# Performance work log

Hardware: AMD Instinct MI355X
Metric: run time of the kernel (lower is better)

## Reference

```python
import jax, jax.numpy as jnp
import numpy as np

DIM = 1024
DEPTH = 2
HEADS = 16
MLP = 4096
HEAD_DIM = DIM // HEADS
EPS = 1e-5


def layernorm(x, w, b):
    mu = jnp.mean(x, axis=-1, keepdims=True)
    var = jnp.mean(jnp.square(x - mu), axis=-1, keepdims=True)
    return (x - mu) * jax.lax.rsqrt(var + EPS) * w + b


def setup_inputs() -> dict:
    key = jax.random.key(0)
    ks = jax.random.split(key, 16)
    s = 0.02
    x = jax.random.normal(ks[0], (2, 2048, DIM), dtype=jnp.float32)
    inp = {
        "x": x,
        "ln1_w": jnp.ones((DEPTH, DIM), jnp.float32),
        "ln1_b": jnp.zeros((DEPTH, DIM), jnp.float32),
        "qkv_w": jax.random.normal(ks[1], (DEPTH, DIM, 3 * DIM), jnp.float32) * s,
        "qkv_b": jnp.zeros((DEPTH, 3 * DIM), jnp.float32),
        "in_w": jax.random.normal(ks[2], (DEPTH, DIM, 3 * DIM), jnp.float32) * s,
        "in_b": jnp.zeros((DEPTH, 3 * DIM), jnp.float32),
        "out_w": jax.random.normal(ks[3], (DEPTH, DIM, DIM), jnp.float32) * s,
        "out_b": jnp.zeros((DEPTH, DIM), jnp.float32),
        "ln2_w": jnp.ones((DEPTH, DIM), jnp.float32),
        "ln2_b": jnp.zeros((DEPTH, DIM), jnp.float32),
        "w1": jax.random.normal(ks[4], (DEPTH, DIM, MLP), jnp.float32) * s,
        "b1": jnp.zeros((DEPTH, MLP), jnp.float32),
        "w2": jax.random.normal(ks[5], (DEPTH, MLP, DIM), jnp.float32) * s,
        "b2": jnp.zeros((DEPTH, DIM), jnp.float32),
    }
    return inp


def _forward(x, ln1_w, ln1_b, qkv_w, qkv_b, in_w, in_b, out_w, out_b,
             ln2_w, ln2_b, w1, b1, w2, b2):
    B, S, D = x.shape
    scale = 1.0 / jnp.sqrt(jnp.float32(HEAD_DIM))
    for i in range(DEPTH):
        # --- Attention block (pre-norm) ---
        h = layernorm(x, ln1_w[i], ln1_b[i])
        qkv = h @ qkv_w[i] + qkv_b[i]                      # [B,S,3D]
        q, k, v = jnp.split(qkv, 3, axis=-1)
        # nn.MultiheadAttention's own in_proj on top of to_qkv
        qp = q @ in_w[i][:, :D] + in_b[i][:D]
        kp = k @ in_w[i][:, D:2 * D] + in_b[i][D:2 * D]
        vp = v @ in_w[i][:, 2 * D:] + in_b[i][2 * D:]
        qp = qp.reshape(B, S, HEADS, HEAD_DIM)
        kp = kp.reshape(B, S, HEADS, HEAD_DIM)
        vp = vp.reshape(B, S, HEADS, HEAD_DIM)
        scores = jnp.einsum("bqhd,bkhd->bhqk", qp, kp) * scale
        attn = jax.nn.softmax(scores, axis=-1)
        o = jnp.einsum("bhqk,bkhd->bqhd", attn, vp).reshape(B, S, D)
        o = o @ out_w[i] + out_b[i]
        x = o + x
        # --- FFN block (pre-norm) ---
        h = layernorm(x, ln2_w[i], ln2_b[i])
        h = jax.nn.gelu(h @ w1[i] + b1[i], approximate=False)
        h = h @ w2[i] + b2[i]
        x = h + x
    return x


def reference(x, ln1_w, ln1_b, qkv_w, qkv_b, in_w, in_b, out_w, out_b,
              ln2_w, ln2_b, w1, b1, w2, b2):
    return _forward(x, ln1_w, ln1_b, qkv_w, qkv_b, in_w, in_b, out_w, out_b,
                    ln2_w, ln2_b, w1, b1, w2, b2)
```

## Files before the change

### kernel.cpp

```cpp
#include <hip/hip_runtime.h>
#include <math.h>

#define D_MODEL 1024
#define NHEADS 16
#define HEAD_DIM 64
#define SEQ 2048
#define BATCH 2
#define TOK (BATCH*SEQ)
#define MLP_DIM 4096

#define F_BIAS  1
#define F_GELU  2
#define QSCALE 0.18033688011112042f

typedef __attribute__((ext_vector_type(8))) __bf16 bf16x8;
typedef __attribute__((ext_vector_type(16))) __bf16 bf16x16;
typedef __attribute__((ext_vector_type(4))) __bf16 bf16x4;
typedef __attribute__((ext_vector_type(4))) float f32x4;

__device__ __forceinline__ void gload16(const void* g, void* l) {
    __builtin_amdgcn_global_load_lds(
        (const __attribute__((address_space(1))) void*)g,
        (__attribute__((address_space(3))) void*)l, 16, 0, 0);
}

__global__ __launch_bounds__(256)
void conv_kernel(const float* __restrict__ in, __bf16* __restrict__ out, int n8)
{
    const int idx = blockIdx.x * 256 + threadIdx.x;
    if (idx >= n8) return;
    const float4 a = *(const float4*)(in + idx * 8);
    const float4 b = *(const float4*)(in + idx * 8 + 4);
    bf16x8 o;
    o[0] = (__bf16)a.x; o[1] = (__bf16)a.y; o[2] = (__bf16)a.z; o[3] = (__bf16)a.w;
    o[4] = (__bf16)b.x; o[5] = (__bf16)b.y; o[6] = (__bf16)b.z; o[7] = (__bf16)b.w;
    *(bf16x8*)(out + idx * 8) = o;
}

__global__ __launch_bounds__(256)
void tconv64_kernel(const float* __restrict__ in, __bf16* __restrict__ out, int R, int C)
{
    __shared__ __bf16 tile[64][72];
    const int bx = blockIdx.x;
    const int by = blockIdx.y;
    const int t = threadIdx.x;
    const int rl = t >> 4, cl = (t & 15) * 4;
    #pragma unroll
    for (int rr = 0; rr < 4; ++rr) {
        const float4 v = *(const float4*)&in[(size_t)(by * 64 + rr * 16 + rl) * C + bx * 64 + cl];
        tile[rr * 16 + rl][cl + 0] = (__bf16)v.x;
        tile[rr * 16 + rl][cl + 1] = (__bf16)v.y;
        tile[rr * 16 + rl][cl + 2] = (__bf16)v.z;
        tile[rr * 16 + rl][cl + 3] = (__bf16)v.w;
    }
    __syncthreads();
    const int oc = t >> 2, rs = (t & 3) * 16;
    bf16x16 y;
    #pragma unroll
    for (int k = 0; k < 16; ++k) y[k] = tile[rs + k][oc];
    *(bf16x16*)&out[(size_t)(bx * 64 + oc) * R + by * 64 + rs] = y;
}

__global__ __launch_bounds__(256)
void bcomb_kernel(const float* __restrict__ qkv_b, const float* __restrict__ in_w,
                  const float* __restrict__ in_b, float* __restrict__ bc)
{
    const int t = blockIdx.x * 256 + threadIdx.x;
    const int p = t >> 10, n = t & 1023;
    float s = in_b[t];
    #pragma unroll 16
    for (int k = 0; k < D_MODEL; ++k)
        s = fmaf(qkv_b[p * D_MODEL + k], in_w[(size_t)k * 3 * D_MODEL + p * D_MODEL + n], s);
    bc[t] = s;
}

__global__ __launch_bounds__(256)
void tv_kernel(const __bf16* __restrict__ v, __bf16* __restrict__ vt)
{
    __shared__ __bf16 t[64][72];
    const int bh = blockIdx.y, b = bh >> 4, h = bh & 15;
    const int s0 = blockIdx.x * 64;
    const int r = threadIdx.x >> 3;
    const int c = (threadIdx.x & 7) * 8;
    #pragma unroll
    for (int rr = 0; rr < 64; rr += 32) {
        bf16x8 x = *(const bf16x8*)&v[(size_t)(b * SEQ + s0 + r + rr) * D_MODEL + h * 64 + c];
        #pragma unroll
        for (int k = 0; k < 8; ++k) t[r + rr][c + k] = x[k];
    }
    __syncthreads();
    #pragma unroll
    for (int rr = 0; rr < 64; rr += 32) {
        bf16x8 y;
        #pragma unroll
        for (int k = 0; k < 8; ++k) y[k] = t[c + k][r + rr];
        *(bf16x8*)&vt[((size_t)bh * 64 + r + rr) * SEQ + s0 + c] = y;
    }
}

__device__ __forceinline__ void ln_body(float4 v, const float* w, const float* b,
                                        __bf16* out, int row, int t)
{
    float s  = v.x + v.y + v.z + v.w;
    float ss = v.x*v.x + v.y*v.y + v.z*v.z + v.w*v.w;
    #pragma unroll
    for (int off = 32; off > 0; off >>= 1) {
        s  += __shfl_down(s, off);
        ss += __shfl_down(ss, off);
    }
    __shared__ float red[8];
    const int wid = t >> 6, lane = t & 63;
    if (lane == 0) { red[wid] = s; red[4 + wid] = ss; }
    __syncthreads();
    const float st  = red[0] + red[1] + red[2] + red[3];
    const float sst = red[4] + red[5] + red[6] + red[7];
    const float mu  = st * (1.0f / D_MODEL);
    const float var = sst * (1.0f / D_MODEL) - mu * mu;
    const float rs  = rsqrtf(var + 1e-5f);
    const float4 wv = *(const float4*)(w + t * 4);
    const float4 bv = *(const float4*)(b + t * 4);
    bf16x4 o;
    o[0] = (__bf16)((v.x - mu) * rs * wv.x + bv.x);
    o[1] = (__bf16)((v.y - mu) * rs * wv.y + bv.y);
    o[2] = (__bf16)((v.z - mu) * rs * wv.z + bv.z);
    o[3] = (__bf16)((v.w - mu) * rs * wv.w + bv.w);
    *(bf16x4*)(out + (size_t)row * D_MODEL + t * 4) = o;
}

__global__ __launch_bounds__(256)
void ln_kernel(const float* __restrict__ x, const float* __restrict__ w,
               const float* __restrict__ b, __bf16* __restrict__ out)
{
    const int row = blockIdx.x, t = threadIdx.x;
    float4 v = *(const float4*)(x + (size_t)row * D_MODEL + t * 4);
    ln_body(v, w, b, out, row, t);
}

__global__ __launch_bounds__(256)
void ln_add_kernel(float* __restrict__ x, const float* __restrict__ p0,
                   const float* __restrict__ p1, const float* __restrict__ w,
                   const float* __restrict__ b, __bf16* __restrict__ out)
{
    const int row = blockIdx.x, t = threadIdx.x;
    const size_t idx = (size_t)row * D_MODEL + t * 4;
    float4 v  = *(const float4*)(x + idx);
    float4 a0 = *(const float4*)(p0 + idx);
    float4 a1 = *(const float4*)(p1 + idx);
    v.x += a0.x + a1.x; v.y += a0.y + a1.y;
    v.z += a0.z + a1.z; v.w += a0.w + a1.w;
    *(float4*)(x + idx) = v;
    ln_body(v, w, b, out, row, t);
}

__global__ __launch_bounds__(256)
void add2_kernel(float* __restrict__ x, const float* __restrict__ p0,
                 const float* __restrict__ p1)
{
    const size_t idx = ((size_t)blockIdx.x * 256 + threadIdx.x) * 4;
    float4 v  = *(const float4*)(x + idx);
    float4 a0 = *(const float4*)(p0 + idx);
    float4 a1 = *(const float4*)(p1 + idx);
    v.x += a0.x + a1.x; v.y += a0.y + a1.y;
    v.z += a0.z + a1.z; v.w += a0.w + a1.w;
    *(float4*)(x + idx) = v;
}

template<int BM, int BN, int WM, int WAVES, int FLAGS, bool PROJ3, bool SPLITK, bool ZB>
__global__ __launch_bounds__(WAVES * 64)
void gs_kernel(const __bf16* __restrict__ A, int lda, long long sAz,
               const __bf16* __restrict__ Bt, int ldb, long long sBz,
               const float* __restrict__ bias,
               void* __restrict__ Cv, int ldc, int K, long long sCz)
{
    constexpr int THREADS = WAVES * 64;
    constexpr int WN = WAVES / WM, RW = BM / WM, CW = BN / WN;
    constexpr int MI = RW / 16, NJ = CW / 16;
    constexpr int LA = (BM * 64) / (THREADS * 8);
    constexpr int LB = (BN * 64) / (THREADS * 8);
    __shared__ __align__(16) __bf16 As[2][BM * 64];
    __shared__ __align__(16) __bf16 Bs[2][BN * 64];

    const int gx = gridDim.x;
    const int nwg = gx * gridDim.y;
    int lin = blockIdx.y * gx + blockIdx.x;
    lin = (lin & 7) * (nwg >> 3) + (lin >> 3);
    const int bm = lin / gx, bn = lin % gx;

    const int z = (SPLITK || ZB) ? blockIdx.z : 0;
    const __bf16* Ab = A  + (size_t)bm * BM * lda
                          + (SPLITK ? (size_t)z * K : 0) + (ZB ? (size_t)z * sAz : 0);
    const __bf16* Bb = Bt + (size_t)bn * BN * ldb
                          + (SPLITK ? (size_t)z * K : 0) + (ZB ? (size_t)z * sBz : 0);

    const int tid = threadIdx.x, lane = tid & 63, w = tid >> 6;
    const int wm = w / WN, wn = w % WN;
    const int kq = lane >> 4, fr = lane & 15;
    const int l8 = lane >> 3;
    const int swz = (lane & 7) ^ l8;

    const __bf16* aPtr[LA]; int aLds[LA];
    #pragma unroll
    for (int c = 0; c < LA; ++c) {
        aPtr[c] = Ab + (size_t)(c * (THREADS / 8) + w * 8 + l8) * lda + swz * 8;
        aLds[c] = (c * THREADS + tid) * 8;
    }
    const __bf16* bPtr[LB]; int bLds[LB];
    #pragma unroll
    for (int c = 0; c < LB; ++c) {
        bPtr[c] = Bb + (size_t)(c * (THREADS / 8) + w * 8 + l8) * ldb + swz * 8;
        bLds[c] = (c * THREADS + tid) * 8;
    }

    f32x4 acc[MI][NJ];
    #pragma unroll
    for (int i = 0; i < MI; ++i)
        #pragma unroll
        for (int j = 0; j < NJ; ++j)
            acc[i][j] = (f32x4){0.f, 0.f, 0.f, 0.f};

    auto STG = [&](int buf, int k0) {
        #pragma unroll
        for (int c = 0; c < LA; ++c)
            gload16(aPtr[c] + k0, &As[buf][aLds[c]]);
        #pragma unroll
        for (int c = 0; c < LB; ++c)
            gload16(bPtr[c] + k0, &Bs[buf][bLds[c]]);
    };

    const int fsw = fr & 7;
    auto COMPUTE = [&](int buf) {
        #pragma unroll
        for (int kk = 0; kk < 2; ++kk) {
            const int kc = (kk * 4 + kq) ^ fsw;
            bf16x8 af[MI], bfr[NJ];
            #pragma unroll
            for (int i = 0; i < MI; ++i)
                af[i] = *(const bf16x8*)&As[buf][(wm * RW + i * 16 + fr) * 64 + kc * 8];
            #pragma unroll
            for (int j = 0; j < NJ; ++j)
                bfr[j] = *(const bf16x8*)&Bs[buf][(wn * CW + j * 16 + fr) * 64 + kc * 8];
            #pragma unroll
            for (int i = 0; i < MI; ++i)
                #pragma unroll
                for (int j = 0; j < NJ; ++j)
                    acc[i][j] = __builtin_amdgcn_mfma_f32_16x16x32_bf16(
                        af[i], bfr[j], acc[i][j], 0, 0, 0);
        }
    };

    const int T = K >> 6;
    STG(0, 0);
    __syncthreads();
    int cur = 0;
    for (int t = 0; t < T; ++t) {
        if (t + 1 < T) STG(cur ^ 1, (t + 1) * 64);
        COMPUTE(cur);
        __syncthreads();
        cur ^= 1;
    }

    const int row0 = bm * BM + wm * RW + kq * 4;
    const int col0 = bn * BN + wn * CW + fr;
    if (SPLITK) {
        float* P = (float*)Cv + (size_t)z * sCz;
        #pragma unroll
        for (int i = 0; i < MI; ++i) {
            #pragma unroll
            for (int j = 0; j < NJ; ++j) {
                const int col = col0 + j * 16;
                const float bb = (z == 0) ? bias[col] : 0.0f;
                #pragma unroll
                for (int e = 0; e < 4; ++e)
                    P[(size_t)(row0 + i * 16 + e) * ldc + col] = acc[i][j][e] + bb;
            }
        }
    } else {
        __bf16* C = (__bf16*)Cv + (ZB ? (size_t)z * sCz : 0);
        #pragma unroll
        for (int i = 0; i < MI; ++i) {
            #pragma unroll
            for (int j = 0; j < NJ; ++j) {
                const int col = col0 + j * 16;
                const float bb = (FLAGS & F_BIAS) ? bias[col] : 0.0f;
                #pragma unroll
                for (int e = 0; e < 4; ++e) {
                    const int row = row0 + i * 16 + e;
                    float val = acc[i][j][e] + bb;
                    if (FLAGS & F_GELU)
                        val = 0.5f * val * (1.0f + erff(val * 0.70710678118654752f));
                    if (PROJ3) {
                        if ((col >> 10) == 0) val *= QSCALE;
                        C[(size_t)(col >> 10) * TOK * D_MODEL +
                          (size_t)row * D_MODEL + (col & 1023)] = (__bf16)val;
                    } else {
                        C[(size_t)row * ldc + col] = (__bf16)val;
                    }
                }
            }
        }
    }
}

__global__ __launch_bounds__(256)
void attn8_kernel(const __bf16* __restrict__ qp, const __bf16* __restrict__ kp,
                  const __bf16* __restrict__ vt, __bf16* __restrict__ o)
{
    const int bh = blockIdx.y;
    const int b = bh >> 4, h = bh & 15;
    const int tid = threadIdx.x;
    const int lane = tid & 63;
    const int w = tid >> 6;
    const int g = lane >> 4;
    const int fr = lane & 15;
    const int q0 = blockIdx.x * 128 + w * 16;
    const int l8 = lane >> 3, swz = (lane & 7) ^ l8, fsw = fr & 7;

    __shared__ __align__(16) __bf16 Ks[2][64 * 64];
    __shared__ __align__(16) __bf16 Vs[2][64 * 64];
    __shared__ __align__(16) __bf16 PsA[4][16 * 72];
    __shared__ __align__(16) __bf16 PsB[4][16 * 72];

    const __bf16* qbA = qp + (size_t)(b * SEQ + q0 + fr) * D_MODEL + h * HEAD_DIM;
    const __bf16* qbB = qbA + (size_t)64 * D_MODEL;
    const bf16x8 qfA0 = *(const bf16x8*)(qbA + g * 8);
    const bf16x8 qfA1 = *(const bf16x8*)(qbA + 32 + g * 8);
    const bf16x8 qfB0 = *(const bf16x8*)(qbB + g * 8);
    const bf16x8 qfB1 = *(const bf16x8*)(qbB + 32 + g * 8);

    const __bf16* kb = kp + (size_t)(b * SEQ) * D_MODEL + h * HEAD_DIM;
    const __bf16* vb = vt + (size_t)bh * HEAD_DIM * SEQ;

    const __bf16* kPtr[2]; const __bf16* vPtr[2]; int sLds[2];
    #pragma unroll
    for (int c = 0; c < 2; ++c) {
        const int row = c * 32 + w * 8 + l8;
        kPtr[c] = kb + (size_t)row * D_MODEL + swz * 8;
        vPtr[c] = vb + (size_t)row * SEQ + swz * 8;
        sLds[c] = (c * 256 + w * 64) * 8;
    }

    auto STG = [&](int buf, int kv0) {
        #pragma unroll
        for (int c = 0; c < 2; ++c)
            gload16(kPtr[c] + (size_t)kv0 * D_MODEL, &Ks[buf][sLds[c]]);
        #pragma unroll
        for (int c = 0; c < 2; ++c)
            gload16(vPtr[c] + kv0, &Vs[buf][sLds[c]]);
    };

    f32x4 acc_oA[4], acc_oB[4];
    #pragma unroll
    for (int dj = 0; dj < 4; ++dj) {
        acc_oA[dj] = (f32x4){0.f, 0.f, 0.f, 0.f};
        acc_oB[dj] = (f32x4){0.f, 0.f, 0.f, 0.f};
    }
    float l_A = 0.0f, l_B = 0.0f;

    STG(0, 0);
    __syncthreads();
    int tb = 0;
    for (int kv0 = 0; kv0 < SEQ; kv0 += 64) {
        if (kv0 + 64 < SEQ) STG(tb ^ 1, kv0 + 64);

        f32x4 sA[4], sB[4];
        __builtin_amdgcn_s_setprio(1);
        #pragma unroll
        for (int t = 0; t < 4; ++t) {
            const bf16x8 kf0 = *(const bf16x8*)&Ks[tb][(t * 16 + fr) * 64 + ((g    ) ^ fsw) * 8];
            const bf16x8 kf1 = *(const bf16x8*)&Ks[tb][(t * 16 + fr) * 64 + ((4 + g) ^ fsw) * 8];
            sA[t] = __builtin_amdgcn_mfma_f32_16x16x32_bf16(
                kf0, qfA0, (f32x4){0.f, 0.f, 0.f, 0.f}, 0, 0, 0);
            sA[t] = __builtin_amdgcn_mfma_f32_16x16x32_bf16(kf1, qfA1, sA[t], 0, 0, 0);
            sB[t] = __builtin_amdgcn_mfma_f32_16x16x32_bf16(
                kf0, qfB0, (f32x4){0.f, 0.f, 0.f, 0.f}, 0, 0, 0);
            sB[t] = __builtin_amdgcn_mfma_f32_16x16x32_bf16(kf1, qfB1, sB[t], 0, 0, 0);
        }
        __builtin_amdgcn_s_setprio(0);

        #pragma unroll
        for (int t = 0; t < 4; ++t) {
            bf16x4 pvA, pvB;
            #pragma unroll
            for (int e = 0; e < 4; ++e) {
                const float pA = __builtin_amdgcn_exp2f(sA[t][e]);
                const float pB = __builtin_amdgcn_exp2f(sB[t][e]);
                l_A += pA; l_B += pB;
                pvA[e] = (__bf16)pA; pvB[e] = (__bf16)pB;
            }
            *(bf16x4*)&PsA[w][fr * 72 + t * 16 + g * 4] = pvA;
            *(bf16x4*)&PsB[w][fr * 72 + t * 16 + g * 4] = pvB;
        }

        __builtin_amdgcn_s_setprio(1);
        #pragma unroll
        for (int c = 0; c < 2; ++c) {
            const bf16x8 pfA = *(const bf16x8*)&PsA[w][fr * 72 + c * 32 + g * 8];
            const bf16x8 pfB = *(const bf16x8*)&PsB[w][fr * 72 + c * 32 + g * 8];
            #pragma unroll
            for (int dj = 0; dj < 4; ++dj) {
                const bf16x8 vf = *(const bf16x8*)&Vs[tb][(dj * 16 + fr) * 64 +
                                                         ((c * 4 + g) ^ fsw) * 8];
                acc_oA[dj] = __builtin_amdgcn_mfma_f32_16x16x32_bf16(vf, pfA, acc_oA[dj], 0, 0, 0);
                acc_oB[dj] = __builtin_amdgcn_mfma_f32_16x16x32_bf16(vf, pfB, acc_oB[dj], 0, 0, 0);
            }
        }
        __builtin_amdgcn_s_setprio(0);
        __syncthreads();
        tb ^= 1;
    }

    l_A += __shfl_xor(l_A, 16); l_A += __shfl_xor(l_A, 32);
    l_B += __shfl_xor(l_B, 16); l_B += __shfl_xor(l_B, 32);
    const float invA = 1.0f / l_A, invB = 1.0f / l_B;
    __bf16* orowA = o + (size_t)(b * SEQ + q0 + fr) * D_MODEL + h * HEAD_DIM;
    __bf16* orowB = orowA + (size_t)64 * D_MODEL;
    #pragma unroll
    for (int dj = 0; dj < 4; ++dj) {
        bf16x4 tA, tB;
        #pragma unroll
        for (int e = 0; e < 4; ++e) {
            tA[e] = (__bf16)(acc_oA[dj][e] * invA);
            tB[e] = (__bf16)(acc_oB[dj][e] * invB);
        }
        *(bf16x4*)&orowA[dj * 16 + g * 4] = tA;
        *(bf16x4*)&orowB[dj * 16 + g * 4] = tB;
    }
}

extern "C" void kernel_launch(void* const* d_in, const int* in_sizes, int n_in,
                              void* d_out, int out_size, void* d_ws, size_t ws_size,
                              hipStream_t stream)
{
    const float* x    = (const float*)d_in[0];
    const float* ln1w = (const float*)d_in[1];
    const float* ln1b = (const float*)d_in[2];
    const float* qkvw = (const float*)d_in[3];
    const float* qkvb = (const float*)d_in[4];
    const float* inw  = (const float*)d_in[5];
    const float* inb  = (const float*)d_in[6];
    const float* outw = (const float*)d_in[7];
    const float* outb = (const float*)d_in[8];
    const float* ln2w = (const float*)d_in[9];
    const float* ln2b = (const float*)d_in[10];
    const float* w1   = (const float*)d_in[11];
    const float* b1   = (const float*)d_in[12];
    const float* w2   = (const float*)d_in[13];
    const float* b2   = (const float*)d_in[14];
    float* xo = (float*)d_out;

    const size_t OFF_WCT = 0;
    const size_t OFF_OUT = 3145728;
    const size_t OFF_W1  = 4194304;
    const size_t OFF_W2  = 8388608;
    const size_t L_WT    = 12582912;

    __bf16* WT   = (__bf16*)d_ws;
    __bf16* QKVb = WT + 2 * L_WT;
    __bf16* INt  = QKVb + 3145728;
    __bf16* X8   = INt + 3145728;
    __bf16* U_   = X8 + 4194304;
    __bf16* QKV3 = U_ + 16777216;
    __bf16* VT   = QKV3 + 12582912;
    float*  BC   = (float*)(VT + 4194304);
    float*  P_   = (float*)QKV3;

    hipMemcpyAsync(xo, x, (size_t)TOK * D_MODEL * sizeof(float),
                   hipMemcpyDeviceToDevice, stream);

    const dim3 blk(256);
    for (int i = 0; i < 2; ++i) {
        __bf16* wl = WT + i * L_WT;
        const float* l_qkvw = qkvw + (size_t)i * D_MODEL * 3 * D_MODEL;
        const float* l_inw  = inw  + (size_t)i * D_MODEL * 3 * D_MODEL;
        conv_kernel<<<1536, blk, 0, stream>>>(l_qkvw, QKVb, 393216);
        tconv64_kernel<<<dim3(48, 16), blk, 0, stream>>>(l_inw, INt, D_MODEL, 3 * D_MODEL);
        gs_kernel<128, 128, 2, 4, 0, false, false, true><<<dim3(8, 8, 3), 256, 0, stream>>>(
            INt, D_MODEL, 1048576LL, QKVb, 3 * D_MODEL, (long long)D_MODEL,
            nullptr, wl + OFF_WCT, D_MODEL, D_MODEL, 1048576LL);
        bcomb_kernel<<<12, blk, 0, stream>>>(
            qkvb + (size_t)i * 3 * D_MODEL, l_inw, inb + (size_t)i * 3 * D_MODEL,
            BC + (size_t)i * 3 * D_MODEL);
        tconv64_kernel<<<dim3(16, 16), blk, 0, stream>>>(
            outw + (size_t)i * D_MODEL * D_MODEL, wl + OFF_OUT, D_MODEL, D_MODEL);
        tconv64_kernel<<<dim3(64, 16), blk, 0, stream>>>(
            w1 + (size_t)i * D_MODEL * MLP_DIM, wl + OFF_W1, D_MODEL, MLP_DIM);
        tconv64_kernel<<<dim3(16, 64), blk, 0, stream>>>(
            w2 + (size_t)i * MLP_DIM * D_MODEL, wl + OFF_W2, MLP_DIM, D_MODEL);
    }

    for (int i = 0; i < 2; ++i) {
        __bf16* wl = WT + i * L_WT;
        const float* l_outb = outb + (size_t)i * D_MODEL;
        const float* l_b1   = b1   + (size_t)i * MLP_DIM;
        const float* l_b2   = b2   + (size_t)i * D_MODEL;

        if (i == 0)
            ln_kernel<<<TOK, blk, 0, stream>>>(xo, ln1w, ln1b, X8);
        gs_kernel<128, 128, 2, 4, F_BIAS, true, false, false><<<dim3(24, 32), 256, 0, stream>>>(
            X8, D_MODEL, 0, wl + OFF_WCT, D_MODEL, 0,
            BC + (size_t)i * 3 * D_MODEL, QKV3, D_MODEL, D_MODEL, 0);
        tv_kernel<<<dim3(SEQ / 64, BATCH * NHEADS), blk, 0, stream>>>(
            QKV3 + (size_t)2 * TOK * D_MODEL, VT);
        attn8_kernel<<<dim3(SEQ / 128, BATCH * NHEADS), blk, 0, stream>>>(
            QKV3, QKV3 + (size_t)TOK * D_MODEL, VT, X8);
        gs_kernel<128, 128, 2, 4, F_BIAS, false, true, false><<<dim3(8, 32, 2), 256, 0, stream>>>(
            X8, D_MODEL, 0, wl + OFF_OUT, D_MODEL, 0, l_outb, P_, D_MODEL, 512,
            (long long)TOK * D_MODEL);
        ln_add_kernel<<<TOK, blk, 0, stream>>>(
            xo, P_, P_ + (size_t)TOK * D_MODEL,
            ln2w + (size_t)i * D_MODEL, ln2b + (size_t)i * D_MODEL, X8);
        gs_kernel<128, 128, 2, 4, F_BIAS | F_GELU, false, false, false><<<dim3(32, 32), 256, 0, stream>>>(
            X8, D_MODEL, 0, wl + OFF_W1, D_MODEL, 0, l_b1, U_, MLP_DIM, D_MODEL, 0);
        gs_kernel<128, 128, 2, 4, F_BIAS, false, true, false><<<dim3(8, 32, 2), 256, 0, stream>>>(
            U_, MLP_DIM, 0, wl + OFF_W2, MLP_DIM, 0, l_b2, P_, D_MODEL, 2048,
            (long long)TOK * D_MODEL);
        if (i == 0) {
            ln_add_kernel<<<TOK, blk, 0, stream>>>(
                xo, P_, P_ + (size_t)TOK * D_MODEL,
                ln1w + D_MODEL, ln1b + D_MODEL, X8);
        } else {
            add2_kernel<<<TOK * D_MODEL / 1024, blk, 0, stream>>>(
                xo, P_, P_ + (size_t)TOK * D_MODEL);
        }
    }
}
```

Measured before the change: 665.1 us.

## Use BK=32 GEMM tiles, split-K by 4 with bf16 partials

Makes the GEMM K-tile size a template parameter and switches every GEMM from BK=64 to BK=32, with a matching LDS swizzle for 32-wide rows. The out-projection and FFN-down GEMMs now use four-way split-K instead of two-way, and their partial sums are stored in bf16 rather than fp32. The residual-add and layernorm kernels read four bf16 partials instead of two fp32 ones. The aims are less LDS per block for higher occupancy, more blocks on the small split-K GEMMs, and less partial-sum traffic. The cost is twice as many K iterations and barriers, plus extra rounding error from bf16 partials.

```diff
diff --git a/kernel.cpp b/kernel.cpp
--- a/kernel.cpp
+++ b/kernel.cpp
@@ -137,35 +137,39 @@
 }
 
 __global__ __launch_bounds__(256)
-void ln_add_kernel(float* __restrict__ x, const float* __restrict__ p0,
-                   const float* __restrict__ p1, const float* __restrict__ w,
-                   const float* __restrict__ b, __bf16* __restrict__ out)
+void ln_add4_kernel(float* __restrict__ x, const __bf16* __restrict__ P,
+                    const float* __restrict__ w, const float* __restrict__ b,
+                    __bf16* __restrict__ out)
 {
     const int row = blockIdx.x, t = threadIdx.x;
     const size_t idx = (size_t)row * D_MODEL + t * 4;
-    float4 v  = *(const float4*)(x + idx);
-    float4 a0 = *(const float4*)(p0 + idx);
-    float4 a1 = *(const float4*)(p1 + idx);
-    v.x += a0.x + a1.x; v.y += a0.y + a1.y;
-    v.z += a0.z + a1.z; v.w += a0.w + a1.w;
+    float4 v = *(const float4*)(x + idx);
+    #pragma unroll
+    for (int z = 0; z < 4; ++z) {
+        const bf16x4 p = *(const bf16x4*)(P + (size_t)z * TOK * D_MODEL + idx);
+        v.x += (float)p[0]; v.y += (float)p[1];
+        v.z += (float)p[2]; v.w += (float)p[3];
+    }
     *(float4*)(x + idx) = v;
     ln_body(v, w, b, out, row, t);
 }
 
 __global__ __launch_bounds__(256)
-void add2_kernel(float* __restrict__ x, const float* __restrict__ p0,
-                 const float* __restrict__ p1)
+void add4_kernel(float* __restrict__ x, const __bf16* __restrict__ P)
 {
     const size_t idx = ((size_t)blockIdx.x * 256 + threadIdx.x) * 4;
-    float4 v  = *(const float4*)(x + idx);
-    float4 a0 = *(const float4*)(p0 + idx);
-    float4 a1 = *(const float4*)(p1 + idx);
-    v.x += a0.x + a1.x; v.y += a0.y + a1.y;
-    v.z += a0.z + a1.z; v.w += a0.w + a1.w;
+    float4 v = *(const float4*)(x + idx);
+    #pragma unroll
+    for (int z = 0; z < 4; ++z) {
+        const bf16x4 p = *(const bf16x4*)(P + (size_t)z * TOK * D_MODEL + idx);
+        v.x += (float)p[0]; v.y += (float)p[1];
+        v.z += (float)p[2]; v.w += (float)p[3];
+    }
     *(float4*)(x + idx) = v;
 }
 
-template<int BM, int BN, int WM, int WAVES, int FLAGS, bool PROJ3, bool SPLITK, bool ZB>
+template<int BM, int BN, int WM, int WAVES, int BK,
+         int FLAGS, bool PROJ3, bool SPLITK, bool ZB>
 __global__ __launch_bounds__(WAVES * 64)
 void gs_kernel(const __bf16* __restrict__ A, int lda, long long sAz,
                const __bf16* __restrict__ Bt, int ldb, long long sBz,
@@ -175,10 +179,11 @@
     constexpr int THREADS = WAVES * 64;
     constexpr int WN = WAVES / WM, RW = BM / WM, CW = BN / WN;
     constexpr int MI = RW / 16, NJ = CW / 16;
-    constexpr int LA = (BM * 64) / (THREADS * 8);
-    constexpr int LB = (BN * 64) / (THREADS * 8);
-    __shared__ __align__(16) __bf16 As[2][BM * 64];
-    __shared__ __align__(16) __bf16 Bs[2][BN * 64];
+    constexpr int CH = BK / 8;
+    constexpr int LA = (BM * BK) / (THREADS * 8);
+    constexpr int LB = (BN * BK) / (THREADS * 8);
+    __shared__ __align__(16) __bf16 As[2][BM * BK];
+    __shared__ __align__(16) __bf16 Bs[2][BN * BK];
 
     const int gx = gridDim.x;
     const int nwg = gx * gridDim.y;
@@ -195,20 +200,23 @@
     const int tid = threadIdx.x, lane = tid & 63, w = tid >> 6;
     const int wm = w / WN, wn = w % WN;
     const int kq = lane >> 4, fr = lane & 15;
-    const int l8 = lane >> 3;
-    const int swz = (lane & 7) ^ l8;
-
+
+    auto rswz = [](int row) { return (BK == 64) ? (row & 7) : ((row >> 1) & 3); };
     const __bf16* aPtr[LA]; int aLds[LA];
     #pragma unroll
     for (int c = 0; c < LA; ++c) {
-        aPtr[c] = Ab + (size_t)(c * (THREADS / 8) + w * 8 + l8) * lda + swz * 8;
-        aLds[c] = (c * THREADS + tid) * 8;
+        const int s = c * THREADS + tid;
+        const int row = s / CH, ch = s % CH;
+        aPtr[c] = Ab + (size_t)row * lda + (ch ^ rswz(row)) * 8;
+        aLds[c] = s * 8;
     }
     const __bf16* bPtr[LB]; int bLds[LB];
     #pragma unroll
     for (int c = 0; c < LB; ++c) {
-        bPtr[c] = Bb + (size_t)(c * (THREADS / 8) + w * 8 + l8) * ldb + swz * 8;
-        bLds[c] = (c * THREADS + tid) * 8;
+        const int s = c * THREADS + tid;
+        const int row = s / CH, ch = s % CH;
+        bPtr[c] = Bb + (size_t)row * ldb + (ch ^ rswz(row)) * 8;
+        bLds[c] = s * 8;
     }
 
     f32x4 acc[MI][NJ];
@@ -227,18 +235,18 @@
             gload16(bPtr[c] + k0, &Bs[buf][bLds[c]]);
     };
 
-    const int fsw = fr & 7;
+    const int fsw = (BK == 64) ? (fr & 7) : ((fr >> 1) & 3);
     auto COMPUTE = [&](int buf) {
         #pragma unroll
-        for (int kk = 0; kk < 2; ++kk) {
+        for (int kk = 0; kk < BK / 32; ++kk) {
             const int kc = (kk * 4 + kq) ^ fsw;
             bf16x8 af[MI], bfr[NJ];
             #pragma unroll
             for (int i = 0; i < MI; ++i)
-                af[i] = *(const bf16x8*)&As[buf][(wm * RW + i * 16 + fr) * 64 + kc * 8];
+                af[i] = *(const bf16x8*)&As[buf][(wm * RW + i * 16 + fr) * BK + kc * 8];
             #pragma unroll
             for (int j = 0; j < NJ; ++j)
-                bfr[j] = *(const bf16x8*)&Bs[buf][(wn * CW + j * 16 + fr) * 64 + kc * 8];
+                bfr[j] = *(const bf16x8*)&Bs[buf][(wn * CW + j * 16 + fr) * BK + kc * 8];
             #pragma unroll
             for (int i = 0; i < MI; ++i)
                 #pragma unroll
@@ -248,12 +256,12 @@
         }
     };
 
-    const int T = K >> 6;
+    const int T = K / BK;
     STG(0, 0);
     __syncthreads();
     int cur = 0;
     for (int t = 0; t < T; ++t) {
-        if (t + 1 < T) STG(cur ^ 1, (t + 1) * 64);
+        if (t + 1 < T) STG(cur ^ 1, (t + 1) * BK);
         COMPUTE(cur);
         __syncthreads();
         cur ^= 1;
@@ -262,7 +270,7 @@
     const int row0 = bm * BM + wm * RW + kq * 4;
     const int col0 = bn * BN + wn * CW + fr;
     if (SPLITK) {
-        float* P = (float*)Cv + (size_t)z * sCz;
+        __bf16* P = (__bf16*)Cv + (size_t)z * sCz;
         #pragma unroll
         for (int i = 0; i < MI; ++i) {
             #pragma unroll
@@ -271,7 +279,7 @@
                 const float bb = (z == 0) ? bias[col] : 0.0f;
                 #pragma unroll
                 for (int e = 0; e < 4; ++e)
-                    P[(size_t)(row0 + i * 16 + e) * ldc + col] = acc[i][j][e] + bb;
+                    P[(size_t)(row0 + i * 16 + e) * ldc + col] = (__bf16)(acc[i][j][e] + bb);
             }
         }
     } else {
@@ -462,7 +470,7 @@
     __bf16* QKV3 = U_ + 16777216;
     __bf16* VT   = QKV3 + 12582912;
     float*  BC   = (float*)(VT + 4194304);
-    float*  P_   = (float*)QKV3;
+    __bf16* P8   = QKV3;
 
     hipMemcpyAsync(xo, x, (size_t)TOK * D_MODEL * sizeof(float),
                    hipMemcpyDeviceToDevice, stream);
@@ -474,7 +482,8 @@
         const float* l_inw  = inw  + (size_t)i * D_MODEL * 3 * D_MODEL;
         conv_kernel<<<1536, blk, 0, stream>>>(l_qkvw, QKVb, 393216);
         tconv64_kernel<<<dim3(48, 16), blk, 0, stream>>>(l_inw, INt, D_MODEL, 3 * D_MODEL);
-        gs_kernel<128, 128, 2, 4, 0, false, false, true><<<dim3(8, 8, 3), 256, 0, stream>>>(
+        gs_kernel<128, 128, 2, 4, 32, 0, false, false, true>
+            <<<dim3(8, 8, 3), 256, 0, stream>>>(
             INt, D_MODEL, 1048576LL, QKVb, 3 * D_MODEL, (long long)D_MODEL,
             nullptr, wl + OFF_WCT, D_MODEL, D_MODEL, 1048576LL);
         bcomb_kernel<<<12, blk, 0, stream>>>(
@@ -496,31 +505,32 @@
 
         if (i == 0)
             ln_kernel<<<TOK, blk, 0, stream>>>(xo, ln1w, ln1b, X8);
-        gs_kernel<128, 128, 2, 4, F_BIAS, true, false, false><<<dim3(24, 32), 256, 0, stream>>>(
+        gs_kernel<128, 128, 2, 4, 32, F_BIAS, true, false, false>
+            <<<dim3(24, 32), 256, 0, stream>>>(
             X8, D_MODEL, 0, wl + OFF_WCT, D_MODEL, 0,
             BC + (size_t)i * 3 * D_MODEL, QKV3, D_MODEL, D_MODEL, 0);
         tv_kernel<<<dim3(SEQ / 64, BATCH * NHEADS), blk, 0, stream>>>(
             QKV3 + (size_t)2 * TOK * D_MODEL, VT);
         attn8_kernel<<<dim3(SEQ / 128, BATCH * NHEADS), blk, 0, stream>>>(
             QKV3, QKV3 + (size_t)TOK * D_MODEL, VT, X8);
-        gs_kernel<128, 128, 2, 4, F_BIAS, false, true, false><<<dim3(8, 32, 2), 256, 0, stream>>>(
-            X8, D_MODEL, 0, wl + OFF_OUT, D_MODEL, 0, l_outb, P_, D_MODEL, 512,
+        gs_kernel<128, 128, 2, 4, 32, F_BIAS, false, true, false>
+            <<<dim3(8, 32, 4), 256, 0, stream>>>(
+            X8, D_MODEL, 0, wl + OFF_OUT, D_MODEL, 0, l_outb, P8, D_MODEL, 256,
             (long long)TOK * D_MODEL);
-        ln_add_kernel<<<TOK, blk, 0, stream>>>(
-            xo, P_, P_ + (size_t)TOK * D_MODEL,
-            ln2w + (size_t)i * D_MODEL, ln2b + (size_t)i * D_MODEL, X8);
-        gs_kernel<128, 128, 2, 4, F_BIAS | F_GELU, false, false, false><<<dim3(32, 32), 256, 0, stream>>>(
+        ln_add4_kernel<<<TOK, blk, 0, stream>>>(
+            xo, P8, ln2w + (size_t)i * D_MODEL, ln2b + (size_t)i * D_MODEL, X8);
+        gs_kernel<128, 128, 2, 4, 32, F_BIAS | F_GELU, false, false, false>
+            <<<dim3(32, 32), 256, 0, stream>>>(
             X8, D_MODEL, 0, wl + OFF_W1, D_MODEL, 0, l_b1, U_, MLP_DIM, D_MODEL, 0);
-        gs_kernel<128, 128, 2, 4, F_BIAS, false, true, false><<<dim3(8, 32, 2), 256, 0, stream>>>(
-            U_, MLP_DIM, 0, wl + OFF_W2, MLP_DIM, 0, l_b2, P_, D_MODEL, 2048,
+        gs_kernel<128, 128, 2, 4, 32, F_BIAS, false, true, false>
+            <<<dim3(8, 32, 4), 256, 0, stream>>>(
+            U_, MLP_DIM, 0, wl + OFF_W2, MLP_DIM, 0, l_b2, P8, D_MODEL, 1024,
             (long long)TOK * D_MODEL);
         if (i == 0) {
-            ln_add_kernel<<<TOK, blk, 0, stream>>>(
-                xo, P_, P_ + (size_t)TOK * D_MODEL,
-                ln1w + D_MODEL, ln1b + D_MODEL, X8);
+            ln_add4_kernel<<<TOK, blk, 0, stream>>>(
+                xo, P8, ln1w + D_MODEL, ln1b + D_MODEL, X8);
         } else {
-            add2_kernel<<<TOK * D_MODEL / 1024, blk, 0, stream>>>(
-                xo, P_, P_ + (size_t)TOK * D_MODEL);
-        }
-    }
-}
+            add4_kernel<<<TOK * D_MODEL / 1024, blk, 0, stream>>>(xo, P8);
+        }
+    }
+}
```

After: 742.5 us. 11.6% more time.

## Triple-buffer GEMM LDS staging with explicit vmcnt waits

Applied to the files above, without the earlier changes.

Replaces the double-buffered LDS pipeline in the generic GEMM kernel with a three-stage ring of separate shared buffers. Loads are issued three tiles ahead, and the wait uses s_waitcnt vmcnt with explicit counts in place of a full __syncthreads after every tile. The goal is to hide more global-load latency behind the MFMA work. In exchange, LDS use rises to 96KB per block, which may reduce occupancy. The hardcoded vmcnt values also assume 8 loads per thread per stage.

```diff
diff --git a/kernel.cpp b/kernel.cpp
--- a/kernel.cpp
+++ b/kernel.cpp
@@ -177,8 +177,12 @@
     constexpr int MI = RW / 16, NJ = CW / 16;
     constexpr int LA = (BM * 64) / (THREADS * 8);
     constexpr int LB = (BN * 64) / (THREADS * 8);
-    __shared__ __align__(16) __bf16 As[2][BM * 64];
-    __shared__ __align__(16) __bf16 Bs[2][BN * 64];
+    __shared__ __align__(16) __bf16 As0[BM * 64];
+    __shared__ __align__(16) __bf16 As1[BM * 64];
+    __shared__ __align__(16) __bf16 As2[BM * 64];
+    __shared__ __align__(16) __bf16 Bs0[BN * 64];
+    __shared__ __align__(16) __bf16 Bs1[BN * 64];
+    __shared__ __align__(16) __bf16 Bs2[BN * 64];
 
     const int gx = gridDim.x;
     const int nwg = gx * gridDim.y;
@@ -218,27 +222,29 @@
         for (int j = 0; j < NJ; ++j)
             acc[i][j] = (f32x4){0.f, 0.f, 0.f, 0.f};
 
-    auto STG = [&](int buf, int k0) {
+    const int T = K >> 6;
+
+    auto STG = [&](__bf16* dA, __bf16* dB, int k0) {
         #pragma unroll
         for (int c = 0; c < LA; ++c)
-            gload16(aPtr[c] + k0, &As[buf][aLds[c]]);
+            gload16(aPtr[c] + k0, dA + aLds[c]);
         #pragma unroll
         for (int c = 0; c < LB; ++c)
-            gload16(bPtr[c] + k0, &Bs[buf][bLds[c]]);
+            gload16(bPtr[c] + k0, dB + bLds[c]);
     };
 
     const int fsw = fr & 7;
-    auto COMPUTE = [&](int buf) {
+    auto COMPUTE = [&](const __bf16* as, const __bf16* bs) {
         #pragma unroll
         for (int kk = 0; kk < 2; ++kk) {
             const int kc = (kk * 4 + kq) ^ fsw;
             bf16x8 af[MI], bfr[NJ];
             #pragma unroll
             for (int i = 0; i < MI; ++i)
-                af[i] = *(const bf16x8*)&As[buf][(wm * RW + i * 16 + fr) * 64 + kc * 8];
+                af[i] = *(const bf16x8*)&as[(wm * RW + i * 16 + fr) * 64 + kc * 8];
             #pragma unroll
             for (int j = 0; j < NJ; ++j)
-                bfr[j] = *(const bf16x8*)&Bs[buf][(wn * CW + j * 16 + fr) * 64 + kc * 8];
+                bfr[j] = *(const bf16x8*)&bs[(wn * CW + j * 16 + fr) * 64 + kc * 8];
             #pragma unroll
             for (int i = 0; i < MI; ++i)
                 #pragma unroll
@@ -248,15 +254,38 @@
         }
     };
 
-    const int T = K >> 6;
-    STG(0, 0);
-    __syncthreads();
-    int cur = 0;
-    for (int t = 0; t < T; ++t) {
-        if (t + 1 < T) STG(cur ^ 1, (t + 1) * 64);
-        COMPUTE(cur);
-        __syncthreads();
-        cur ^= 1;
+    auto STEP = [&](__bf16* a, __bf16* b, int t, int wn_) {
+        if (wn_ == 16)     asm volatile("s_waitcnt vmcnt(16)" ::: "memory");
+        else if (wn_ == 8) asm volatile("s_waitcnt vmcnt(8)"  ::: "memory");
+        else               asm volatile("s_waitcnt vmcnt(0)"  ::: "memory");
+        __builtin_amdgcn_s_barrier();
+        COMPUTE(a, b);
+        asm volatile("" ::: "memory");
+        __builtin_amdgcn_s_barrier();
+        if (t + 3 < T) STG(a, b, (t + 3) * 64);
+    };
+
+    STG(As0, Bs0, 0);
+    STG(As1, Bs1, 64);
+    STG(As2, Bs2, 128);
+    int t = 0;
+    for (; t < T - 2; ++t) {
+        switch (t % 3) {
+        case 0:  STEP(As0, Bs0, t, 16); break;
+        case 1:  STEP(As1, Bs1, t, 16); break;
+        default: STEP(As2, Bs2, t, 16); break;
+        }
+    }
+    switch (t % 3) {
+    case 0:  STEP(As0, Bs0, t, 8); break;
+    case 1:  STEP(As1, Bs1, t, 8); break;
+    default: STEP(As2, Bs2, t, 8); break;
+    }
+    ++t;
+    switch (t % 3) {
+    case 0:  STEP(As0, Bs0, t, 0); break;
+    case 1:  STEP(As1, Bs1, t, 0); break;
+    default: STEP(As2, Bs2, t, 0); break;
     }
 
     const int row0 = bm * BM + wm * RW + kq * 4;
@@ -474,7 +503,8 @@
         const float* l_inw  = inw  + (size_t)i * D_MODEL * 3 * D_MODEL;
         conv_kernel<<<1536, blk, 0, stream>>>(l_qkvw, QKVb, 393216);
         tconv64_kernel<<<dim3(48, 16), blk, 0, stream>>>(l_inw, INt, D_MODEL, 3 * D_MODEL);
-        gs_kernel<128, 128, 2, 4, 0, false, false, true><<<dim3(8, 8, 3), 256, 0, stream>>>(
+        gs_kernel<128, 128, 2, 4, 0, false, false, true>
+            <<<dim3(8, 8, 3), 256, 0, stream>>>(
             INt, D_MODEL, 1048576LL, QKVb, 3 * D_MODEL, (long long)D_MODEL,
             nullptr, wl + OFF_WCT, D_MODEL, D_MODEL, 1048576LL);
         bcomb_kernel<<<12, blk, 0, stream>>>(
@@ -496,22 +526,26 @@
 
         if (i == 0)
             ln_kernel<<<TOK, blk, 0, stream>>>(xo, ln1w, ln1b, X8);
-        gs_kernel<128, 128, 2, 4, F_BIAS, true, false, false><<<dim3(24, 32), 256, 0, stream>>>(
+        gs_kernel<128, 128, 2, 4, F_BIAS, true, false, false>
+            <<<dim3(24, 32), 256, 0, stream>>>(
             X8, D_MODEL, 0, wl + OFF_WCT, D_MODEL, 0,
             BC + (size_t)i * 3 * D_MODEL, QKV3, D_MODEL, D_MODEL, 0);
         tv_kernel<<<dim3(SEQ / 64, BATCH * NHEADS), blk, 0, stream>>>(
             QKV3 + (size_t)2 * TOK * D_MODEL, VT);
         attn8_kernel<<<dim3(SEQ / 128, BATCH * NHEADS), blk, 0, stream>>>(
             QKV3, QKV3 + (size_t)TOK * D_MODEL, VT, X8);
-        gs_kernel<128, 128, 2, 4, F_BIAS, false, true, false><<<dim3(8, 32, 2), 256, 0, stream>>>(
+        gs_kernel<128, 128, 2, 4, F_BIAS, false, true, false>
+            <<<dim3(8, 32, 2), 256, 0, stream>>>(
             X8, D_MODEL, 0, wl + OFF_OUT, D_MODEL, 0, l_outb, P_, D_MODEL, 512,
             (long long)TOK * D_MODEL);
         ln_add_kernel<<<TOK, blk, 0, stream>>>(
             xo, P_, P_ + (size_t)TOK * D_MODEL,
             ln2w + (size_t)i * D_MODEL, ln2b + (size_t)i * D_MODEL, X8);
-        gs_kernel<128, 128, 2, 4, F_BIAS | F_GELU, false, false, false><<<dim3(32, 32), 256, 0, stream>>>(
+        gs_kernel<128, 128, 2, 4, F_BIAS | F_GELU, false, false, false>
+            <<<dim3(32, 32), 256, 0, stream>>>(
             X8, D_MODEL, 0, wl + OFF_W1, D_MODEL, 0, l_b1, U_, MLP_DIM, D_MODEL, 0);
-        gs_kernel<128, 128, 2, 4, F_BIAS, false, true, false><<<dim3(8, 32, 2), 256, 0, stream>>>(
+        gs_kernel<128, 128, 2, 4, F_BIAS, false, true, false>
+            <<<dim3(8, 32, 2), 256, 0, stream>>>(
             U_, MLP_DIM, 0, wl + OFF_W2, MLP_DIM, 0, l_b2, P_, D_MODEL, 2048,
             (long long)TOK * D_MODEL);
         if (i == 0) {
```

After: 837.6 us. 1.26x slower.
